# Kernel optimization log

Measured on AMD Instinct MI355X. Metric: run time of the kernel, lower is better.

Reference implementation:

```python
import jax, jax.numpy as jnp
import numpy as np

B = 4096  # number of graphs (segments)
H = 256   # hidden_aff = hidden_comp = hidden_prot
NEG = -1e30

def leaky(x):
    return jax.nn.leaky_relu(x, 0.1)

def _lin(key, fin, fout):
    k1, k2 = jax.random.split(key)
    lim = 1.0 / np.sqrt(fin)
    W = jax.random.uniform(k1, (fin, fout), jnp.float32, -lim, lim)
    b = jax.random.uniform(k2, (fout,), jnp.float32, -lim, lim)
    return W, b

def setup_inputs() -> dict:
    key = jax.random.key(0)
    ks = jax.random.split(key, 16)
    N = 262144
    comp_feature = jax.random.normal(ks[0], (N, H), jnp.float32)
    prot_feature = jax.random.normal(ks[1], (N, H), jnp.float32)
    batch_comp = jnp.sort(jax.random.randint(ks[2], (N,), 0, B, jnp.int32))
    batch_prot = jnp.sort(jax.random.randint(ks[3], (N,), 0, B, jnp.int32))
    c_aff_W, c_aff_b = _lin(ks[4], H, H)
    c_sup_W, c_sup_b = _lin(ks[5], H, H)
    p_aff_W, p_aff_b = _lin(ks[6], H, H)
    raw_W1, raw_b1 = _lin(ks[7], 3 * H, H)
    raw_W2, raw_b2 = _lin(ks[8], H, H)
    alpha_W1, alpha_b1 = _lin(ks[9], 3 * H, H)
    alpha_W2, alpha_b2 = _lin(ks[10], H, 1)
    out_W1, out_b1 = _lin(ks[11], H, H)
    out_W2, out_b2 = _lin(ks[12], H, 1)
    return dict(comp_feature=comp_feature, prot_feature=prot_feature,
                batch_comp=batch_comp, batch_prot=batch_prot,
                c_aff_W=c_aff_W, c_aff_b=c_aff_b, c_sup_W=c_sup_W, c_sup_b=c_sup_b,
                p_aff_W=p_aff_W, p_aff_b=p_aff_b,
                raw_W1=raw_W1, raw_b1=raw_b1, raw_W2=raw_W2, raw_b2=raw_b2,
                alpha_W1=alpha_W1, alpha_b1=alpha_b1, alpha_W2=alpha_W2, alpha_b2=alpha_b2,
                out_W1=out_W1, out_b1=out_b1, out_W2=out_W2, out_b2=out_b2)

def reference(comp_feature, prot_feature, batch_comp, batch_prot,
              c_aff_W, c_aff_b, c_sup_W, c_sup_b, p_aff_W, p_aff_b,
              raw_W1, raw_b1, raw_W2, raw_b2,
              alpha_W1, alpha_b1, alpha_W2, alpha_b2,
              out_W1, out_b1, out_W2, out_b2):
    comp_emb = leaky(comp_feature @ c_aff_W + c_aff_b)           # [N, H]
    prot_emb = leaky(prot_feature @ p_aff_W + p_aff_b)           # [N, H]
    prot_pool = jax.ops.segment_max(prot_emb, batch_prot, num_segments=B)  # [B, H]
    supe = jax.ops.segment_sum(leaky(comp_feature @ c_sup_W + c_sup_b),
                               batch_comp, num_segments=B)       # [B, H]
    feat = jnp.concatenate([comp_emb, supe[batch_comp], prot_pool[batch_comp]], axis=1)  # [N, 3H]
    raw = leaky(feat @ raw_W1 + raw_b1) @ raw_W2 + raw_b2        # [N, H]
    prealpha = leaky(feat @ alpha_W1 + alpha_b1) @ alpha_W2 + alpha_b2  # [N, 1]
    # scatter softmax over graphs
    seg_max = jax.ops.segment_max(prealpha, batch_comp, num_segments=B)
    a_exp = jnp.exp(prealpha - seg_max[batch_comp])
    a_sum = jax.ops.segment_sum(a_exp, batch_comp, num_segments=B) + 1e-6
    alpha = a_exp / a_sum[batch_comp]                            # [N, 1]
    vector = jax.ops.segment_sum(raw * alpha, batch_comp, num_segments=B)  # [B, H]
    affinity_pred = leaky(vector @ out_W1 + out_b1) @ out_W2 + out_b2      # [B, 1]
    return vector, alpha, affinity_pred
```

## Files before the change

kernel.cpp:

```cpp
#include <hip/hip_runtime.h>
#include <cstddef>
#include <cstdint>

#define HDIM 256
#define BSEG 4096

typedef __bf16 bf16x8 __attribute__((ext_vector_type(8)));
typedef float f32x4 __attribute__((ext_vector_type(4)));

__device__ __forceinline__ float leaky(float x) { return x >= 0.f ? x : 0.1f * x; }
__device__ __forceinline__ float bf2f(ushort u) {
    return __builtin_bit_cast(float, (uint32_t)u << 16);
}
__device__ __forceinline__ ushort f2bf(float f) {
    uint32_t x = __builtin_bit_cast(uint32_t, f);
    return (ushort)((x + 0x7fffu + ((x >> 16) & 1u)) >> 16);
}
__device__ __forceinline__ bf16x8 pack8(float4 a, float4 b) {
    union { ushort s[8]; bf16x8 v; } u;
    u.s[0] = f2bf(a.x); u.s[1] = f2bf(a.y); u.s[2] = f2bf(a.z); u.s[3] = f2bf(a.w);
    u.s[4] = f2bf(b.x); u.s[5] = f2bf(b.y); u.s[6] = f2bf(b.z); u.s[7] = f2bf(b.w);
    return u.v;
}
__device__ __forceinline__ void store_bf4(ushort* p, float v0, float v1, float v2, float v3) {
    ushort4 o; o.x = f2bf(v0); o.y = f2bf(v1); o.z = f2bf(v2); o.w = f2bf(v3);
    *(ushort4*)p = o;
}

__device__ __forceinline__ void gld16(const ushort* g, ushort* lds) {
    __builtin_amdgcn_global_load_lds(
        (const __attribute__((address_space(1))) uint32_t*)g,
        (__attribute__((address_space(3))) uint32_t*)lds, 16, 0, 0);
}

__global__ void seg_bounds_k(const int* __restrict__ bc, const int* __restrict__ bp,
                             int* __restrict__ sc, int* __restrict__ sp, int n, int nb)
{
    int t = blockIdx.x * blockDim.x + threadIdx.x;
    if (t >= 2 * (nb + 1)) return;
    bool isc = (t <= nb);
    const int* a = isc ? bc : bp;
    int v = isc ? t : t - (nb + 1);
    int lo = 0, hi = n;
    while (lo < hi) { int mid = (lo + hi) >> 1; if (a[mid] < v) lo = mid + 1; else hi = mid; }
    if (isc) sc[t] = lo; else sp[t - (nb + 1)] = lo;
}

__global__ __launch_bounds__(256) void wt_cast_all(
    const float* __restrict__ s0, const float* __restrict__ s1,
    const float* __restrict__ s2, const float* __restrict__ s3,
    const float* __restrict__ s4,
    ushort* __restrict__ d0, ushort* __restrict__ d1, ushort* __restrict__ d2,
    ushort* __restrict__ d3, ushort* __restrict__ d4)
{
    int m = blockIdx.x >> 4, tile = blockIdx.x & 15;
    const float* s = m == 0 ? s0 : m == 1 ? s1 : m == 2 ? s2 : m == 3 ? s3 : s4;
    ushort*      d = m == 0 ? d0 : m == 1 ? d1 : m == 2 ? d2 : m == 3 ? d3 : d4;
    int r0 = (tile >> 2) * 64, c0 = (tile & 3) * 64;
    __shared__ ushort t[64][72];
    int cc = threadIdx.x & 63, rr = threadIdx.x >> 6;
    for (int r = rr; r < 64; r += 4) t[cc][r] = f2bf(s[(size_t)(r0 + r) * 256 + c0 + cc]);
    __syncthreads();
    for (int r = rr; r < 64; r += 4) d[(size_t)(c0 + r) * 256 + r0 + cc] = t[r][cc];
}

template<bool LEAKYACT, bool ROWBIAS, bool AFP32, bool ALPHADOT, int YT>
__global__ __launch_bounds__(512) void mg3(
    const void* __restrict__ Av, const ushort* __restrict__ WT,
    const float* __restrict__ bias0, const float* __restrict__ bias1,
    const float* __restrict__ rt0, const float* __restrict__ rt1,
    const int* __restrict__ idx,
    ushort* __restrict__ out0, ushort* __restrict__ out1,
    const float* __restrict__ w2, float* __restrict__ pre)
{
    __shared__ __attribute__((aligned(16))) ushort Bs[2][256 * 32];
    __shared__ __attribute__((aligned(16))) ushort As[2][128 * 32];
    __shared__ float pb[128][4];

    const int tid = threadIdx.x;
    const int l = tid & 63, w = tid >> 6;

    const uint nwg = gridDim.x, orig = blockIdx.x;
    const uint swz = (orig & 7) * (nwg >> 3) + (orig >> 3);
    const int bx = (int)(swz / YT), cb = (int)(swz % YT);
    const int row0 = bx * 128, colb = cb * 256;

    const float*  Af = (const float*)Av;
    const ushort* Ah = (const ushort*)Av;

    const int sB0 = w * 128 + l;
    const int rB0 = sB0 >> 2,        rB1 = (sB0 + 64) >> 2;
    const int qB0 = (sB0 & 3) ^ ((rB0 >> 1) & 3), qB1 = ((sB0 + 64) & 3) ^ ((rB1 >> 1) & 3);
    const ushort* srcB0 = WT + (size_t)(colb + rB0) * HDIM + qB0 * 8;
    const ushort* srcB1 = WT + (size_t)(colb + rB1) * HDIM + qB1 * 8;
    const int srow = tid >> 2, sj = tid & 3;
    const int lj = sj ^ ((srow >> 1) & 3);
    const float*  fsrcA = Af + (size_t)(row0 + srow) * HDIM + lj * 8;
    const ushort* hsrcA = Ah + (size_t)(row0 + srow) * HDIM + lj * 8;

    const int wr = (w >> 2) * 64, wc = (w & 3) * 64;
    const int lr = l & 15, lt = l >> 4;

    f32x4 acc[4][4] = {};

#define STAGE_B(buf, k0) do { \
        gld16(srcB0 + (k0), &Bs[buf][sB0 * 8]); \
        gld16(srcB1 + (k0), &Bs[buf][(sB0 + 64) * 8]); \
    } while (0)

#define COMPUTE(buf) do { \
        bf16x8 af[4], bv[4]; \
        _Pragma("unroll") \
        for (int m = 0; m < 4; ++m) { \
            const int row = wr + m * 16 + lr; \
            const int q = lt ^ ((row >> 1) & 3); \
            af[m] = *(const bf16x8*)&As[buf][row * 32 + q * 8]; \
        } \
        _Pragma("unroll") \
        for (int n = 0; n < 4; ++n) { \
            const int brow = wc + n * 16 + lr; \
            const int q = lt ^ ((brow >> 1) & 3); \
            bv[n] = *(const bf16x8*)&Bs[buf][brow * 32 + q * 8]; \
        } \
        _Pragma("unroll") \
        for (int m = 0; m < 4; ++m) \
            _Pragma("unroll") \
            for (int n = 0; n < 4; ++n) \
                acc[m][n] = __builtin_amdgcn_mfma_f32_16x16x32_bf16(bv[n], af[m], acc[m][n], 0, 0, 0); \
    } while (0)

    int cur = 0;
    if (AFP32) {
        float4 av0, av1;
        av0 = *(const float4*)(fsrcA + 0);
        av1 = *(const float4*)(fsrcA + 4);
        STAGE_B(0, 0);
        *(bf16x8*)&As[0][tid * 8] = pack8(av0, av1);
        __syncthreads();
        #pragma unroll
        for (int t = 1; t < 8; ++t) {
            av0 = *(const float4*)(fsrcA + t * 32);
            av1 = *(const float4*)(fsrcA + t * 32 + 4);
            STAGE_B(cur ^ 1, t * 32);
            COMPUTE(cur);
            *(bf16x8*)&As[cur ^ 1][tid * 8] = pack8(av0, av1);
            __syncthreads();
            cur ^= 1;
        }
        COMPUTE(cur);
    } else {
        STAGE_B(0, 0);
        gld16(hsrcA, &As[0][tid * 8]);
        __syncthreads();
        #pragma unroll
        for (int t = 1; t < 8; ++t) {
            STAGE_B(cur ^ 1, t * 32);
            gld16(hsrcA + t * 32, &As[cur ^ 1][tid * 8]);
            COMPUTE(cur);
            __syncthreads();
            cur ^= 1;
        }
        COMPUTE(cur);
    }

#undef STAGE_B
#undef COMPUTE

    if (ALPHADOT && cb == 1) {
        #pragma unroll
        for (int m = 0; m < 4; ++m) {
            const int row = row0 + wr + m * 16 + lr;
            const float* rrow = rt1 + (size_t)idx[row] * HDIM;
            float p = 0.f;
            #pragma unroll
            for (int n = 0; n < 4; ++n) {
                const int c = wc + n * 16 + (lt << 2);
                float4 r4 = *(const float4*)&rrow[c];
                float4 w4 = *(const float4*)&w2[c];
                float v0 = acc[m][n][0] + r4.x, v1 = acc[m][n][1] + r4.y;
                float v2 = acc[m][n][2] + r4.z, v3 = acc[m][n][3] + r4.w;
                if (LEAKYACT) { v0 = leaky(v0); v1 = leaky(v1); v2 = leaky(v2); v3 = leaky(v3); }
                p += v0 * w4.x + v1 * w4.y + v2 * w4.z + v3 * w4.w;
            }
            p += __shfl_xor(p, 16);
            p += __shfl_xor(p, 32);
            if (lt == 0) pb[wr + m * 16 + lr][w & 3] = p;
        }
        __syncthreads();
        if (tid < 128) pre[row0 + tid] = pb[tid][0] + pb[tid][1] + pb[tid][2] + pb[tid][3];
    } else {
        const float* bias = (YT == 2 && cb == 1) ? bias1 : bias0;
        const float* rtab = (YT == 2 && cb == 1) ? rt1 : rt0;
        ushort* outp = (YT == 2 && cb == 1) ? out1 : out0;
        #pragma unroll
        for (int m = 0; m < 4; ++m) {
            const int row = row0 + wr + m * 16 + lr;
            const float* rrow = nullptr;
            if (ROWBIAS) rrow = rtab + (size_t)idx[row] * HDIM;
            #pragma unroll
            for (int n = 0; n < 4; ++n) {
                const int c = wc + n * 16 + (lt << 2);
                float v0 = acc[m][n][0], v1 = acc[m][n][1], v2 = acc[m][n][2], v3 = acc[m][n][3];
                if (bias) {
                    float4 b4 = *(const float4*)&bias[c];
                    v0 += b4.x; v1 += b4.y; v2 += b4.z; v3 += b4.w;
                }
                if (ROWBIAS) {
                    float4 r4 = *(const float4*)&rrow[c];
                    v0 += r4.x; v1 += r4.y; v2 += r4.z; v3 += r4.w;
                }
                if (LEAKYACT) { v0 = leaky(v0); v1 = leaky(v1); v2 = leaky(v2); v3 = leaky(v3); }
                store_bf4(&outp[(size_t)row * HDIM + c], v0, v1, v2, v3);
            }
        }
    }
}

__global__ __launch_bounds__(256) void gemm64_2(
    const float* __restrict__ A, const float* __restrict__ A2,
    const float* __restrict__ Wb_r, const float* __restrict__ Wc_r, const float* __restrict__ bias_r,
    const float* __restrict__ Wb_a, const float* __restrict__ Wc_a, const float* __restrict__ bias_a,
    float* __restrict__ Cr, float* __restrict__ Ca)
{
    const int K = HDIM, NO = HDIM;
    const float* W  = blockIdx.z ? Wb_a : Wb_r;
    const float* W2 = blockIdx.z ? Wc_a : Wc_r;
    const float* bias = blockIdx.z ? bias_a : bias_r;
    float* C = blockIdx.z ? Ca : Cr;

    __shared__ float As [16][68];
    __shared__ float Bs [16][68];
    __shared__ float As2[16][68];
    __shared__ float Bs2[16][68];

    const int tid = threadIdx.x;
    const int tx = tid & 15, ty = tid >> 4;
    const int row0 = blockIdx.x * 64, col0 = blockIdx.y * 64;

    const int lr = tid >> 2;
    const int lk = (tid & 3) << 2;
    const int bk = tid >> 4;
    const int bj = (tid & 15) << 2;

    float acc[4][4] = {};

    for (int k0 = 0; k0 < K; k0 += 16) {
        float4 a4 = *(const float4*)&A[(size_t)(row0 + lr) * K + k0 + lk];
        As[lk + 0][lr] = a4.x; As[lk + 1][lr] = a4.y;
        As[lk + 2][lr] = a4.z; As[lk + 3][lr] = a4.w;
        *(float4*)&Bs[bk][bj] = *(const float4*)&W[(size_t)(k0 + bk) * NO + col0 + bj];
        float4 c4 = *(const float4*)&A2[(size_t)(row0 + lr) * K + k0 + lk];
        As2[lk + 0][lr] = c4.x; As2[lk + 1][lr] = c4.y;
        As2[lk + 2][lr] = c4.z; As2[lk + 3][lr] = c4.w;
        *(float4*)&Bs2[bk][bj] = *(const float4*)&W2[(size_t)(k0 + bk) * NO + col0 + bj];
        __syncthreads();
        #pragma unroll
        for (int kk = 0; kk < 16; ++kk) {
            float4 av = *(const float4*)&As[kk][ty << 2];
            float4 bv = *(const float4*)&Bs[kk][tx << 2];
            float a_[4] = {av.x, av.y, av.z, av.w};
            float b_[4] = {bv.x, bv.y, bv.z, bv.w};
            #pragma unroll
            for (int i = 0; i < 4; ++i)
                #pragma unroll
                for (int j = 0; j < 4; ++j)
                    acc[i][j] += a_[i] * b_[j];
            float4 av2 = *(const float4*)&As2[kk][ty << 2];
            float4 bv2 = *(const float4*)&Bs2[kk][tx << 2];
            float c_[4] = {av2.x, av2.y, av2.z, av2.w};
            float d_[4] = {bv2.x, bv2.y, bv2.z, bv2.w};
            #pragma unroll
            for (int i = 0; i < 4; ++i)
                #pragma unroll
                for (int j = 0; j < 4; ++j)
                    acc[i][j] += c_[i] * d_[j];
        }
        __syncthreads();
    }

    #pragma unroll
    for (int i = 0; i < 4; ++i) {
        int row = row0 + (ty << 2) + i;
        float vv[4];
        #pragma unroll
        for (int j = 0; j < 4; ++j) {
            int col = col0 + (tx << 2) + j;
            vv[j] = acc[i][j] + bias[col];
        }
        float4 o; o.x = vv[0]; o.y = vv[1]; o.z = vv[2]; o.w = vv[3];
        *(float4*)&C[(size_t)row * NO + col0 + (tx << 2)] = o;
    }
}

template<bool ISMAX>
__global__ __launch_bounds__(256) void seg_reduce8(const ushort* __restrict__ in,
        const int* __restrict__ starts, float* __restrict__ out)
{
    __shared__ float part[8][HDIM];
    const int b = blockIdx.x, tid = threadIdx.x;
    const int sub = tid & 31, r = tid >> 5;
    const int s = starts[b], e = starts[b + 1];
    float a[8];
    #pragma unroll
    for (int j = 0; j < 8; ++j) a[j] = ISMAX ? -INFINITY : 0.f;
    for (int i = s + r; i < e; i += 8) {
        uint4 v = *(const uint4*)&in[(size_t)i * HDIM + sub * 8];
        float f[8] = { bf2f((ushort)v.x), bf2f((ushort)(v.x >> 16)),
                       bf2f((ushort)v.y), bf2f((ushort)(v.y >> 16)),
                       bf2f((ushort)v.z), bf2f((ushort)(v.z >> 16)),
                       bf2f((ushort)v.w), bf2f((ushort)(v.w >> 16)) };
        #pragma unroll
        for (int j = 0; j < 8; ++j) a[j] = ISMAX ? fmaxf(a[j], f[j]) : (a[j] + f[j]);
    }
    #pragma unroll
    for (int j = 0; j < 8; ++j) part[r][sub * 8 + j] = a[j];
    __syncthreads();
    float res = part[0][tid];
    #pragma unroll
    for (int j = 1; j < 8; ++j) res = ISMAX ? fmaxf(res, part[j][tid]) : (res + part[j][tid]);
    out[(size_t)b * HDIM + tid] = res;
}

__global__ __launch_bounds__(64) void seg_softmax_k(const float* __restrict__ pre,
        const int* __restrict__ starts, float* __restrict__ alpha, float* __restrict__ sa)
{
    int b = blockIdx.x, lane = threadIdx.x;
    int s = starts[b], e = starts[b + 1];
    float m = -INFINITY;
    for (int i = s + lane; i < e; i += 64) m = fmaxf(m, pre[i]);
    #pragma unroll
    for (int off = 32; off; off >>= 1) m = fmaxf(m, __shfl_xor(m, off));
    float S = 0.f;
    for (int i = s + lane; i < e; i += 64) S += expf(pre[i] - m);
    #pragma unroll
    for (int off = 32; off; off >>= 1) S += __shfl_xor(S, off);
    float denom = S + 1e-6f;
    if (lane == 0) sa[b] = S / denom;
    for (int i = s + lane; i < e; i += 64) alpha[i] = expf(pre[i] - m) / denom;
}

__global__ __launch_bounds__(256) void seg_wsum8(const ushort* __restrict__ raw,
        const float* __restrict__ alpha, const int* __restrict__ starts,
        float* __restrict__ vec)
{
    __shared__ float part[8][HDIM];
    const int b = blockIdx.x, tid = threadIdx.x;
    const int sub = tid & 31, r = tid >> 5;
    const int s = starts[b], e = starts[b + 1];
    float a[8] = {};
    for (int i = s + r; i < e; i += 8) {
        float al = alpha[i];
        uint4 v = *(const uint4*)&raw[(size_t)i * HDIM + sub * 8];
        a[0] += bf2f((ushort)v.x) * al;        a[1] += bf2f((ushort)(v.x >> 16)) * al;
        a[2] += bf2f((ushort)v.y) * al;        a[3] += bf2f((ushort)(v.y >> 16)) * al;
        a[4] += bf2f((ushort)v.z) * al;        a[5] += bf2f((ushort)(v.z >> 16)) * al;
        a[6] += bf2f((ushort)v.w) * al;        a[7] += bf2f((ushort)(v.w >> 16)) * al;
    }
    #pragma unroll
    for (int j = 0; j < 8; ++j) part[r][sub * 8 + j] = a[j];
    __syncthreads();
    float res = 0.f;
    #pragma unroll
    for (int j = 0; j < 8; ++j) res += part[j][tid];
    vec[(size_t)b * HDIM + tid] = res;
}

__global__ __launch_bounds__(256) void final_k(
    const float* __restrict__ hw, const float* __restrict__ sa,
    const float* __restrict__ W2r, const float* __restrict__ rb2,
    const float* __restrict__ oW1, const float* __restrict__ ob1,
    const float* __restrict__ oW2, const float* __restrict__ ob2,
    float* __restrict__ out_vec, float* __restrict__ out_aff)
{
    __shared__ float v[HDIM];
    __shared__ float vecs[HDIM];
    __shared__ float red[4];
    int b = blockIdx.x, t = threadIdx.x;
    v[t] = hw[(size_t)b * HDIM + t];
    __syncthreads();
    float a = rb2[t] * sa[b];
    #pragma unroll 8
    for (int k = 0; k < HDIM; ++k) a += v[k] * W2r[(size_t)k * HDIM + t];
    out_vec[(size_t)b * HDIM + t] = a;
    vecs[t] = a;
    __syncthreads();
    float h = ob1[t];
    #pragma unroll 8
    for (int k = 0; k < HDIM; ++k) h += vecs[k] * oW1[(size_t)k * HDIM + t];
    h = leaky(h);
    float p = h * oW2[t];
    #pragma unroll
    for (int off = 32; off; off >>= 1) p += __shfl_down(p, off);
    int lane = t & 63, wid = t >> 6;
    if (lane == 0) red[wid] = p;
    __syncthreads();
    if (t == 0) out_aff[b] = red[0] + red[1] + red[2] + red[3] + ob2[0];
}

extern "C" void kernel_launch(void* const* d_in, const int* in_sizes, int n_in,
                              void* d_out, int out_size, void* d_ws, size_t ws_size,
                              hipStream_t stream)
{
    const int N = in_sizes[2];
    const int H = HDIM;
    const int B = BSEG;

    const float* comp   = (const float*)d_in[0];
    const float* prot   = (const float*)d_in[1];
    const int*   bc     = (const int*)d_in[2];
    const int*   bp     = (const int*)d_in[3];
    const float* c_aff_W = (const float*)d_in[4];
    const float* c_aff_b = (const float*)d_in[5];
    const float* c_sup_W = (const float*)d_in[6];
    const float* c_sup_b = (const float*)d_in[7];
    const float* p_aff_W = (const float*)d_in[8];
    const float* p_aff_b = (const float*)d_in[9];
    const float* raw_W1  = (const float*)d_in[10];
    const float* raw_b1  = (const float*)d_in[11];
    const float* raw_W2  = (const float*)d_in[12];
    const float* raw_b2  = (const float*)d_in[13];
    const float* alpha_W1 = (const float*)d_in[14];
    const float* alpha_b1 = (const float*)d_in[15];
    const float* alpha_W2 = (const float*)d_in[16];
    const float* out_W1  = (const float*)d_in[18];
    const float* out_b1  = (const float*)d_in[19];
    const float* out_W2  = (const float*)d_in[20];
    const float* out_b2  = (const float*)d_in[21];

    const size_t NBIG = (size_t)N * H;
    const size_t SSEG = (size_t)B * H;

    char* p = (char*)d_ws;
    ushort* e1 = (ushort*)p; p += NBIG * 2;
    ushort* e2 = (ushort*)p; p += NBIG * 2;
    ushort* e3 = (ushort*)p; p += NBIG * 2;
    float* supe = (float*)p;  p += SSEG * 4;
    float* pool = (float*)p;  p += SSEG * 4;
    float* gr   = (float*)p;  p += SSEG * 4;
    float* ga   = (float*)p;  p += SSEG * 4;
    float* hw   = (float*)p;  p += SSEG * 4;
    float* sa   = (float*)p;  p += (size_t)B * 4;
    float* pre  = (float*)p;  p += (size_t)N * 4;
    ushort* WT1 = (ushort*)p; p += (size_t)512 * 256 * 2;
    ushort* WTp = (ushort*)p; p += (size_t)256 * 256 * 2;
    ushort* WT2 = (ushort*)p; p += (size_t)512 * 256 * 2;
    int* sc = (int*)p; p += (size_t)(B + 1) * 4;
    int* sp = (int*)p; p += (size_t)(B + 1) * 4;
    if ((size_t)(p - (char*)d_ws) > ws_size) return;

    ushort* h1 = e3;

    float* out_vec   = (float*)d_out;
    float* out_alpha = out_vec + SSEG;
    float* out_aff   = out_alpha + N;

    dim3 blk(256), blk5(512);

    seg_bounds_k<<<(2 * (B + 1) + 255) / 256, blk, 0, stream>>>(bc, bp, sc, sp, N, B);
    wt_cast_all<<<5 * 16, blk, 0, stream>>>(
        c_aff_W, c_sup_W, p_aff_W, raw_W1, alpha_W1,
        WT1, WT1 + 65536, WTp, WT2, WT2 + 65536);

    mg3<true, false, true, false, 2><<<dim3(N / 128 * 2), blk5, 0, stream>>>(
        comp, WT1, c_aff_b, c_sup_b, nullptr, nullptr, nullptr, e1, e2, nullptr, nullptr);
    mg3<true, false, true, false, 1><<<dim3(N / 128), blk5, 0, stream>>>(
        prot, WTp, p_aff_b, nullptr, nullptr, nullptr, nullptr, e3, nullptr, nullptr, nullptr);
    seg_reduce8<false><<<B, blk, 0, stream>>>(e2, sc, supe);
    seg_reduce8<true ><<<B, blk, 0, stream>>>(e3, sp, pool);
    gemm64_2<<<dim3(B / 64, 4, 2), blk, 0, stream>>>(supe, pool,
        raw_W1 + H * H, raw_W1 + 2 * H * H, raw_b1,
        alpha_W1 + H * H, alpha_W1 + 2 * H * H, alpha_b1, gr, ga);
    mg3<true, true, false, true, 2><<<dim3(N / 128 * 2), blk5, 0, stream>>>(
        e1, WT2, nullptr, nullptr, gr, ga, bc, h1, nullptr, alpha_W2, pre);
    seg_softmax_k<<<B, dim3(64), 0, stream>>>(pre, sc, out_alpha, sa);
    seg_wsum8<<<B, blk, 0, stream>>>(h1, out_alpha, sc, hw);
    final_k<<<B, blk, 0, stream>>>(hw, sa, raw_W2, raw_b2,
        out_W1, out_b1, out_W2, out_b2, out_vec, out_aff);
}
```

Baseline: 686.3 us.

## Merge comp/prot GEMM launches and triple-buffer the K loop with depth-2 prefetch

```diff
diff --git a/kernel.cpp b/kernel.cpp
--- a/kernel.cpp
+++ b/kernel.cpp
@@ -65,16 +65,18 @@
 }
 
 template<bool LEAKYACT, bool ROWBIAS, bool AFP32, bool ALPHADOT, int YT>
-__global__ __launch_bounds__(512) void mg3(
-    const void* __restrict__ Av, const ushort* __restrict__ WT,
+__global__ __launch_bounds__(512) void mg4(
+    const void* __restrict__ Av, const void* __restrict__ Av2,
+    const ushort* __restrict__ WT,
     const float* __restrict__ bias0, const float* __restrict__ bias1,
+    const float* __restrict__ bias2,
     const float* __restrict__ rt0, const float* __restrict__ rt1,
     const int* __restrict__ idx,
-    ushort* __restrict__ out0, ushort* __restrict__ out1,
+    ushort* __restrict__ out0, ushort* __restrict__ out1, ushort* __restrict__ out2,
     const float* __restrict__ w2, float* __restrict__ pre)
 {
-    __shared__ __attribute__((aligned(16))) ushort Bs[2][256 * 32];
-    __shared__ __attribute__((aligned(16))) ushort As[2][128 * 32];
+    __shared__ __attribute__((aligned(16))) ushort Bs[3][256 * 32];
+    __shared__ __attribute__((aligned(16))) ushort As[3][128 * 32];
     __shared__ float pb[128][4];
 
     const int tid = threadIdx.x;
@@ -85,8 +87,9 @@
     const int bx = (int)(swz / YT), cb = (int)(swz % YT);
     const int row0 = bx * 128, colb = cb * 256;
 
-    const float*  Af = (const float*)Av;
-    const ushort* Ah = (const ushort*)Av;
+    const void* Asel = (YT == 3 && cb == 2) ? Av2 : Av;
+    const float*  Af = (const float*)Asel;
+    const ushort* Ah = (const ushort*)Asel;
 
     const int sB0 = w * 128 + l;
     const int rB0 = sB0 >> 2,        rB1 = (sB0 + 64) >> 2;
@@ -102,8 +105,15 @@
     const int lr = l & 15, lt = l >> 4;
 
     f32x4 acc[4][4] = {};
-
-#define STAGE_B(buf, k0) do { \
+    float4 ra[2][2];
+
+#define PREF(buf, k0, slot) do { \
+        if (AFP32) { \
+            ra[slot][0] = *(const float4*)(fsrcA + (k0)); \
+            ra[slot][1] = *(const float4*)(fsrcA + (k0) + 4); \
+        } else { \
+            gld16(hsrcA + (k0), &As[buf][tid * 8]); \
+        } \
         gld16(srcB0 + (k0), &Bs[buf][sB0 * 8]); \
         gld16(srcB1 + (k0), &Bs[buf][(sB0 + 64) * 8]); \
     } while (0)
@@ -129,41 +139,39 @@
                 acc[m][n] = __builtin_amdgcn_mfma_f32_16x16x32_bf16(bv[n], af[m], acc[m][n], 0, 0, 0); \
     } while (0)
 
-    int cur = 0;
+    PREF(0, 0, 0);
+    PREF(1, 32, 1);
     if (AFP32) {
-        float4 av0, av1;
-        av0 = *(const float4*)(fsrcA + 0);
-        av1 = *(const float4*)(fsrcA + 4);
-        STAGE_B(0, 0);
-        *(bf16x8*)&As[0][tid * 8] = pack8(av0, av1);
-        __syncthreads();
-        #pragma unroll
-        for (int t = 1; t < 8; ++t) {
-            av0 = *(const float4*)(fsrcA + t * 32);
-            av1 = *(const float4*)(fsrcA + t * 32 + 4);
-            STAGE_B(cur ^ 1, t * 32);
-            COMPUTE(cur);
-            *(bf16x8*)&As[cur ^ 1][tid * 8] = pack8(av0, av1);
-            __syncthreads();
-            cur ^= 1;
+        asm volatile("s_waitcnt vmcnt(4)" ::: "memory");
+        *(bf16x8*)&As[0][tid * 8] = pack8(ra[0][0], ra[0][1]);
+        asm volatile("s_waitcnt lgkmcnt(0)" ::: "memory");
+    } else {
+        asm volatile("s_waitcnt vmcnt(3)" ::: "memory");
+    }
+    __builtin_amdgcn_s_barrier();
+    __builtin_amdgcn_sched_barrier(0);
+
+    #pragma unroll
+    for (int t = 0; t < 8; ++t) {
+        if (t + 2 < 8) PREF((t + 2) % 3, (t + 2) * 32, t & 1);
+        COMPUTE(t % 3);
+        if (t < 7) {
+            if (t + 2 < 8) {
+                if (AFP32) asm volatile("s_waitcnt vmcnt(4)" ::: "memory");
+                else       asm volatile("s_waitcnt vmcnt(3)" ::: "memory");
+            } else {
+                asm volatile("s_waitcnt vmcnt(0)" ::: "memory");
+            }
+            if (AFP32) {
+                *(bf16x8*)&As[(t + 1) % 3][tid * 8] = pack8(ra[(t + 1) & 1][0], ra[(t + 1) & 1][1]);
+                asm volatile("s_waitcnt lgkmcnt(0)" ::: "memory");
+            }
+            __builtin_amdgcn_s_barrier();
+            __builtin_amdgcn_sched_barrier(0);
         }
-        COMPUTE(cur);
-    } else {
-        STAGE_B(0, 0);
-        gld16(hsrcA, &As[0][tid * 8]);
-        __syncthreads();
-        #pragma unroll
-        for (int t = 1; t < 8; ++t) {
-            STAGE_B(cur ^ 1, t * 32);
-            gld16(hsrcA + t * 32, &As[cur ^ 1][tid * 8]);
-            COMPUTE(cur);
-            __syncthreads();
-            cur ^= 1;
-        }
-        COMPUTE(cur);
-    }
-
-#undef STAGE_B
+    }
+
+#undef PREF
 #undef COMPUTE
 
     if (ALPHADOT && cb == 1) {
@@ -189,9 +197,9 @@
         __syncthreads();
         if (tid < 128) pre[row0 + tid] = pb[tid][0] + pb[tid][1] + pb[tid][2] + pb[tid][3];
     } else {
-        const float* bias = (YT == 2 && cb == 1) ? bias1 : bias0;
-        const float* rtab = (YT == 2 && cb == 1) ? rt1 : rt0;
-        ushort* outp = (YT == 2 && cb == 1) ? out1 : out0;
+        const float* bias = (YT >= 2 && cb == 1) ? bias1 : (YT == 3 && cb == 2) ? bias2 : bias0;
+        ushort* outp      = (YT >= 2 && cb == 1) ? out1  : (YT == 3 && cb == 2) ? out2  : out0;
+        const float* rtab = (cb == 1) ? rt1 : rt0;
         #pragma unroll
         for (int m = 0; m < 4; ++m) {
             const int row = row0 + wr + m * 16 + lr;
@@ -461,17 +469,17 @@
         c_aff_W, c_sup_W, p_aff_W, raw_W1, alpha_W1,
         WT1, WT1 + 65536, WTp, WT2, WT2 + 65536);
 
-    mg3<true, false, true, false, 2><<<dim3(N / 128 * 2), blk5, 0, stream>>>(
-        comp, WT1, c_aff_b, c_sup_b, nullptr, nullptr, nullptr, e1, e2, nullptr, nullptr);
-    mg3<true, false, true, false, 1><<<dim3(N / 128), blk5, 0, stream>>>(
-        prot, WTp, p_aff_b, nullptr, nullptr, nullptr, nullptr, e3, nullptr, nullptr, nullptr);
+    mg4<true, false, true, false, 3><<<dim3(N / 128 * 3), blk5, 0, stream>>>(
+        comp, prot, WT1, c_aff_b, c_sup_b, p_aff_b, nullptr, nullptr, nullptr,
+        e1, e2, e3, nullptr, nullptr);
     seg_reduce8<false><<<B, blk, 0, stream>>>(e2, sc, supe);
     seg_reduce8<true ><<<B, blk, 0, stream>>>(e3, sp, pool);
     gemm64_2<<<dim3(B / 64, 4, 2), blk, 0, stream>>>(supe, pool,
         raw_W1 + H * H, raw_W1 + 2 * H * H, raw_b1,
         alpha_W1 + H * H, alpha_W1 + 2 * H * H, alpha_b1, gr, ga);
-    mg3<true, true, false, true, 2><<<dim3(N / 128 * 2), blk5, 0, stream>>>(
-        e1, WT2, nullptr, nullptr, gr, ga, bc, h1, nullptr, alpha_W2, pre);
+    mg4<true, true, false, true, 2><<<dim3(N / 128 * 2), blk5, 0, stream>>>(
+        e1, nullptr, WT2, nullptr, nullptr, nullptr, gr, ga, bc,
+        h1, nullptr, nullptr, alpha_W2, pre);
     seg_softmax_k<<<B, dim3(64), 0, stream>>>(pre, sc, out_alpha, sa);
     seg_wsum8<<<B, blk, 0, stream>>>(h1, out_alpha, sc, hw);
     final_k<<<B, blk, 0, stream>>>(hw, sa, raw_W2, raw_b2,
```

Result: no change. 695.1 us (+1.3%).

## Stage full-K A tile in LDS and compute all output columns per block

Applied to the files above, without the earlier changes.

```diff
diff --git a/kernel.cpp b/kernel.cpp
--- a/kernel.cpp
+++ b/kernel.cpp
@@ -64,155 +64,148 @@
     for (int r = rr; r < 64; r += 4) d[(size_t)(c0 + r) * 256 + r0 + cc] = t[r][cc];
 }
 
-template<bool LEAKYACT, bool ROWBIAS, bool AFP32, bool ALPHADOT, int YT>
-__global__ __launch_bounds__(512) void mg3(
-    const void* __restrict__ Av, const ushort* __restrict__ WT,
-    const float* __restrict__ bias0, const float* __restrict__ bias1,
+__device__ __forceinline__ void tile_mma(const ushort* As, const ushort* __restrict__ WT,
+        int colT, int lr, int lt, f32x4 acc[4][4])
+{
+    #pragma unroll
+    for (int ks = 0; ks < 8; ++ks) {
+        bf16x8 af[4], bv[4];
+        #pragma unroll
+        for (int m = 0; m < 4; ++m) {
+            const int r = m * 16 + lr;
+            const int c = ks * 4 + lt;
+            af[m] = *(const bf16x8*)&As[(r * 32 + (c ^ (r & 7))) * 8];
+        }
+        #pragma unroll
+        for (int n = 0; n < 4; ++n)
+            bv[n] = *(const bf16x8*)&WT[(size_t)(colT + n * 16 + lr) * HDIM + ks * 32 + lt * 8];
+        #pragma unroll
+        for (int m = 0; m < 4; ++m)
+            #pragma unroll
+            for (int n = 0; n < 4; ++n)
+                acc[m][n] = __builtin_amdgcn_mfma_f32_16x16x32_bf16(bv[n], af[m], acc[m][n], 0, 0, 0);
+    }
+}
+
+template<int MODE>
+__global__ __launch_bounds__(256, 4) void mgs(
+    const float* __restrict__ Ac, const float* __restrict__ Ap,
+    const ushort* __restrict__ Ahb,
+    const ushort* __restrict__ WT,
+    const float* __restrict__ b0, const float* __restrict__ b1, const float* __restrict__ b2,
     const float* __restrict__ rt0, const float* __restrict__ rt1,
     const int* __restrict__ idx,
-    ushort* __restrict__ out0, ushort* __restrict__ out1,
-    const float* __restrict__ w2, float* __restrict__ pre)
-{
-    __shared__ __attribute__((aligned(16))) ushort Bs[2][256 * 32];
-    __shared__ __attribute__((aligned(16))) ushort As[2][128 * 32];
-    __shared__ float pb[128][4];
+    ushort* __restrict__ o0, ushort* __restrict__ o1, ushort* __restrict__ o2,
+    const float* __restrict__ w2, float* __restrict__ pre, int NB)
+{
+    __shared__ __attribute__((aligned(16))) ushort As[64 * 256];
+    __shared__ float pb[64][4];
 
     const int tid = threadIdx.x;
     const int l = tid & 63, w = tid >> 6;
-
-    const uint nwg = gridDim.x, orig = blockIdx.x;
-    const uint swz = (orig & 7) * (nwg >> 3) + (orig >> 3);
-    const int bx = (int)(swz / YT), cb = (int)(swz % YT);
-    const int row0 = bx * 128, colb = cb * 256;
-
-    const float*  Af = (const float*)Av;
-    const ushort* Ah = (const ushort*)Av;
-
-    const int sB0 = w * 128 + l;
-    const int rB0 = sB0 >> 2,        rB1 = (sB0 + 64) >> 2;
-    const int qB0 = (sB0 & 3) ^ ((rB0 >> 1) & 3), qB1 = ((sB0 + 64) & 3) ^ ((rB1 >> 1) & 3);
-    const ushort* srcB0 = WT + (size_t)(colb + rB0) * HDIM + qB0 * 8;
-    const ushort* srcB1 = WT + (size_t)(colb + rB1) * HDIM + qB1 * 8;
-    const int srow = tid >> 2, sj = tid & 3;
-    const int lj = sj ^ ((srow >> 1) & 3);
-    const float*  fsrcA = Af + (size_t)(row0 + srow) * HDIM + lj * 8;
-    const ushort* hsrcA = Ah + (size_t)(row0 + srow) * HDIM + lj * 8;
-
-    const int wr = (w >> 2) * 64, wc = (w & 3) * 64;
     const int lr = l & 15, lt = l >> 4;
 
-    f32x4 acc[4][4] = {};
-
-#define STAGE_B(buf, k0) do { \
-        gld16(srcB0 + (k0), &Bs[buf][sB0 * 8]); \
-        gld16(srcB1 + (k0), &Bs[buf][(sB0 + 64) * 8]); \
-    } while (0)
-
-#define COMPUTE(buf) do { \
-        bf16x8 af[4], bv[4]; \
-        _Pragma("unroll") \
-        for (int m = 0; m < 4; ++m) { \
-            const int row = wr + m * 16 + lr; \
-            const int q = lt ^ ((row >> 1) & 3); \
-            af[m] = *(const bf16x8*)&As[buf][row * 32 + q * 8]; \
-        } \
-        _Pragma("unroll") \
-        for (int n = 0; n < 4; ++n) { \
-            const int brow = wc + n * 16 + lr; \
-            const int q = lt ^ ((brow >> 1) & 3); \
-            bv[n] = *(const bf16x8*)&Bs[buf][brow * 32 + q * 8]; \
-        } \
-        _Pragma("unroll") \
-        for (int m = 0; m < 4; ++m) \
-            _Pragma("unroll") \
-            for (int n = 0; n < 4; ++n) \
-                acc[m][n] = __builtin_amdgcn_mfma_f32_16x16x32_bf16(bv[n], af[m], acc[m][n], 0, 0, 0); \
-    } while (0)
-
-    int cur = 0;
-    if (AFP32) {
-        float4 av0, av1;
-        av0 = *(const float4*)(fsrcA + 0);
-        av1 = *(const float4*)(fsrcA + 4);
-        STAGE_B(0, 0);
-        *(bf16x8*)&As[0][tid * 8] = pack8(av0, av1);
+    const int bid = blockIdx.x;
+    const bool isProt = (MODE == 0) && (bid >= NB);
+    const int row0 = (isProt ? bid - NB : bid) * 64;
+
+    if (MODE == 0) {
+        const float* A = isProt ? Ap : Ac;
+        #pragma unroll
+        for (int i = 0; i < 8; ++i) {
+            const int s = i * 256 + tid;
+            const int r = s >> 5, q = s & 31;
+            const float* src = A + (size_t)(row0 + r) * HDIM + ((q ^ (r & 7)) << 3);
+            float4 x = *(const float4*)src;
+            float4 y = *(const float4*)(src + 4);
+            *(bf16x8*)&As[s * 8] = pack8(x, y);
+        }
+    } else {
+        #pragma unroll
+        for (int i = 0; i < 8; ++i) {
+            const int s = i * 256 + tid;
+            const int r = s >> 5, q = s & 31;
+            gld16(Ahb + (size_t)(row0 + r) * HDIM + ((q ^ (r & 7)) << 3), &As[s * 8]);
+        }
+    }
+    __syncthreads();
+
+    if (MODE == 0) {
+        const int ntile = isProt ? 1 : 2;
+        #pragma unroll
+        for (int t = 0; t < 2; ++t) {
+            if (t >= ntile) break;
+            const int colT = isProt ? (512 + w * 64) : (w * 128 + t * 64);
+            f32x4 acc[4][4] = {};
+            tile_mma(As, WT, colT, lr, lt, acc);
+            const int g = colT >> 8;
+            const float* bias = g == 0 ? b0 : g == 1 ? b1 : b2;
+            ushort* outp      = g == 0 ? o0 : g == 1 ? o1 : o2;
+            const int cin = (colT & 255) + (lt << 2);
+            #pragma unroll
+            for (int m = 0; m < 4; ++m) {
+                const int row = row0 + m * 16 + lr;
+                #pragma unroll
+                for (int n = 0; n < 4; ++n) {
+                    const int c = cin + n * 16;
+                    float4 b4 = *(const float4*)&bias[c];
+                    float v0 = leaky(acc[m][n][0] + b4.x);
+                    float v1 = leaky(acc[m][n][1] + b4.y);
+                    float v2 = leaky(acc[m][n][2] + b4.z);
+                    float v3 = leaky(acc[m][n][3] + b4.w);
+                    store_bf4(&outp[(size_t)row * HDIM + c], v0, v1, v2, v3);
+                }
+            }
+        }
+    } else {
+        {
+            const int colT = w * 64;
+            f32x4 acc[4][4] = {};
+            tile_mma(As, WT, colT, lr, lt, acc);
+            const int cin = colT + (lt << 2);
+            #pragma unroll
+            for (int m = 0; m < 4; ++m) {
+                const int row = row0 + m * 16 + lr;
+                const float* rrow = rt0 + (size_t)idx[row] * HDIM;
+                #pragma unroll
+                for (int n = 0; n < 4; ++n) {
+                    const int c = cin + n * 16;
+                    float4 r4 = *(const float4*)&rrow[c];
+                    float v0 = leaky(acc[m][n][0] + r4.x);
+                    float v1 = leaky(acc[m][n][1] + r4.y);
+                    float v2 = leaky(acc[m][n][2] + r4.z);
+                    float v3 = leaky(acc[m][n][3] + r4.w);
+                    store_bf4(&o0[(size_t)row * HDIM + c], v0, v1, v2, v3);
+                }
+            }
+        }
+        {
+            const int colT = 256 + w * 64;
+            f32x4 acc[4][4] = {};
+            tile_mma(As, WT, colT, lr, lt, acc);
+            const int cin = (colT - 256) + (lt << 2);
+            #pragma unroll
+            for (int m = 0; m < 4; ++m) {
+                const int row = row0 + m * 16 + lr;
+                const float* rrow = rt1 + (size_t)idx[row] * HDIM;
+                float p = 0.f;
+                #pragma unroll
+                for (int n = 0; n < 4; ++n) {
+                    const int c = cin + n * 16;
+                    float4 r4 = *(const float4*)&rrow[c];
+                    float4 w4 = *(const float4*)&w2[c];
+                    p += leaky(acc[m][n][0] + r4.x) * w4.x;
+                    p += leaky(acc[m][n][1] + r4.y) * w4.y;
+                    p += leaky(acc[m][n][2] + r4.z) * w4.z;
+                    p += leaky(acc[m][n][3] + r4.w) * w4.w;
+                }
+                p += __shfl_xor(p, 16);
+                p += __shfl_xor(p, 32);
+                if (lt == 0) pb[m * 16 + lr][w] = p;
+            }
+        }
         __syncthreads();
-        #pragma unroll
-        for (int t = 1; t < 8; ++t) {
-            av0 = *(const float4*)(fsrcA + t * 32);
-            av1 = *(const float4*)(fsrcA + t * 32 + 4);
-            STAGE_B(cur ^ 1, t * 32);
-            COMPUTE(cur);
-            *(bf16x8*)&As[cur ^ 1][tid * 8] = pack8(av0, av1);
-            __syncthreads();
-            cur ^= 1;
-        }
-        COMPUTE(cur);
-    } else {
-        STAGE_B(0, 0);
-        gld16(hsrcA, &As[0][tid * 8]);
-        __syncthreads();
-        #pragma unroll
-        for (int t = 1; t < 8; ++t) {
-            STAGE_B(cur ^ 1, t * 32);
-            gld16(hsrcA + t * 32, &As[cur ^ 1][tid * 8]);
-            COMPUTE(cur);
-            __syncthreads();
-            cur ^= 1;
-        }
-        COMPUTE(cur);
-    }
-
-#undef STAGE_B
-#undef COMPUTE
-
-    if (ALPHADOT && cb == 1) {
-        #pragma unroll
-        for (int m = 0; m < 4; ++m) {
-            const int row = row0 + wr + m * 16 + lr;
-            const float* rrow = rt1 + (size_t)idx[row] * HDIM;
-            float p = 0.f;
-            #pragma unroll
-            for (int n = 0; n < 4; ++n) {
-                const int c = wc + n * 16 + (lt << 2);
-                float4 r4 = *(const float4*)&rrow[c];
-                float4 w4 = *(const float4*)&w2[c];
-                float v0 = acc[m][n][0] + r4.x, v1 = acc[m][n][1] + r4.y;
-                float v2 = acc[m][n][2] + r4.z, v3 = acc[m][n][3] + r4.w;
-                if (LEAKYACT) { v0 = leaky(v0); v1 = leaky(v1); v2 = leaky(v2); v3 = leaky(v3); }
-                p += v0 * w4.x + v1 * w4.y + v2 * w4.z + v3 * w4.w;
-            }
-            p += __shfl_xor(p, 16);
-            p += __shfl_xor(p, 32);
-            if (lt == 0) pb[wr + m * 16 + lr][w & 3] = p;
-        }
-        __syncthreads();
-        if (tid < 128) pre[row0 + tid] = pb[tid][0] + pb[tid][1] + pb[tid][2] + pb[tid][3];
-    } else {
-        const float* bias = (YT == 2 && cb == 1) ? bias1 : bias0;
-        const float* rtab = (YT == 2 && cb == 1) ? rt1 : rt0;
-        ushort* outp = (YT == 2 && cb == 1) ? out1 : out0;
-        #pragma unroll
-        for (int m = 0; m < 4; ++m) {
-            const int row = row0 + wr + m * 16 + lr;
-            const float* rrow = nullptr;
-            if (ROWBIAS) rrow = rtab + (size_t)idx[row] * HDIM;
-            #pragma unroll
-            for (int n = 0; n < 4; ++n) {
-                const int c = wc + n * 16 + (lt << 2);
-                float v0 = acc[m][n][0], v1 = acc[m][n][1], v2 = acc[m][n][2], v3 = acc[m][n][3];
-                if (bias) {
-                    float4 b4 = *(const float4*)&bias[c];
-                    v0 += b4.x; v1 += b4.y; v2 += b4.z; v3 += b4.w;
-                }
-                if (ROWBIAS) {
-                    float4 r4 = *(const float4*)&rrow[c];
-                    v0 += r4.x; v1 += r4.y; v2 += r4.z; v3 += r4.w;
-                }
-                if (LEAKYACT) { v0 = leaky(v0); v1 = leaky(v1); v2 = leaky(v2); v3 = leaky(v3); }
-                store_bf4(&outp[(size_t)row * HDIM + c], v0, v1, v2, v3);
-            }
-        }
+        if (tid < 64) pre[row0 + tid] = pb[tid][0] + pb[tid][1] + pb[tid][2] + pb[tid][3];
     }
 }
 
@@ -454,24 +447,25 @@
     float* out_alpha = out_vec + SSEG;
     float* out_aff   = out_alpha + N;
 
-    dim3 blk(256), blk5(512);
+    dim3 blk(256);
+    const int NB = N / 64;
 
     seg_bounds_k<<<(2 * (B + 1) + 255) / 256, blk, 0, stream>>>(bc, bp, sc, sp, N, B);
     wt_cast_all<<<5 * 16, blk, 0, stream>>>(
         c_aff_W, c_sup_W, p_aff_W, raw_W1, alpha_W1,
         WT1, WT1 + 65536, WTp, WT2, WT2 + 65536);
 
-    mg3<true, false, true, false, 2><<<dim3(N / 128 * 2), blk5, 0, stream>>>(
-        comp, WT1, c_aff_b, c_sup_b, nullptr, nullptr, nullptr, e1, e2, nullptr, nullptr);
-    mg3<true, false, true, false, 1><<<dim3(N / 128), blk5, 0, stream>>>(
-        prot, WTp, p_aff_b, nullptr, nullptr, nullptr, nullptr, e3, nullptr, nullptr, nullptr);
+    mgs<0><<<2 * NB, blk, 0, stream>>>(
+        comp, prot, nullptr, WT1, c_aff_b, c_sup_b, p_aff_b,
+        nullptr, nullptr, nullptr, e1, e2, e3, nullptr, nullptr, NB);
     seg_reduce8<false><<<B, blk, 0, stream>>>(e2, sc, supe);
     seg_reduce8<true ><<<B, blk, 0, stream>>>(e3, sp, pool);
     gemm64_2<<<dim3(B / 64, 4, 2), blk, 0, stream>>>(supe, pool,
         raw_W1 + H * H, raw_W1 + 2 * H * H, raw_b1,
         alpha_W1 + H * H, alpha_W1 + 2 * H * H, alpha_b1, gr, ga);
-    mg3<true, true, false, true, 2><<<dim3(N / 128 * 2), blk5, 0, stream>>>(
-        e1, WT2, nullptr, nullptr, gr, ga, bc, h1, nullptr, alpha_W2, pre);
+    mgs<1><<<NB, blk, 0, stream>>>(
+        nullptr, nullptr, e1, WT2, nullptr, nullptr, nullptr,
+        gr, ga, bc, h1, nullptr, nullptr, alpha_W2, pre, NB);
     seg_softmax_k<<<B, dim3(64), 0, stream>>>(pre, sc, out_alpha, sa);
     seg_wsum8<<<B, blk, 0, stream>>>(h1, out_alpha, sc, hw);
     final_k<<<B, blk, 0, stream>>>(hw, sa, raw_W2, raw_b2,
```

After: 749.7 us. 9.2% more time.

## Prefetch A two stages ahead with manual vmcnt waits in GEMM main loop

Applied to the files above, without the earlier changes.

```diff
diff --git a/kernel.cpp b/kernel.cpp
--- a/kernel.cpp
+++ b/kernel.cpp
@@ -65,7 +65,7 @@
 }
 
 template<bool LEAKYACT, bool ROWBIAS, bool AFP32, bool ALPHADOT, int YT>
-__global__ __launch_bounds__(512) void mg3(
+__global__ __launch_bounds__(512) void mg5(
     const void* __restrict__ Av, const ushort* __restrict__ WT,
     const float* __restrict__ bias0, const float* __restrict__ bias1,
     const float* __restrict__ rt0, const float* __restrict__ rt1,
@@ -102,11 +102,29 @@
     const int lr = l & 15, lt = l >> 4;
 
     f32x4 acc[4][4] = {};
+    float4 fa0[2], fa1[2];
+    bf16x8 ha[2];
 
 #define STAGE_B(buf, k0) do { \
         gld16(srcB0 + (k0), &Bs[buf][sB0 * 8]); \
         gld16(srcB1 + (k0), &Bs[buf][(sB0 + 64) * 8]); \
     } while (0)
+
+#define LOAD_A(slot, k0) do { \
+        if (AFP32) { \
+            fa0[slot] = *(const float4*)(fsrcA + (k0)); \
+            fa1[slot] = *(const float4*)(fsrcA + (k0) + 4); \
+        } else { \
+            ha[slot] = *(const bf16x8*)(hsrcA + (k0)); \
+        } \
+    } while (0)
+
+#define WRITE_A(buf, slot) do { \
+        if (AFP32) *(bf16x8*)&As[buf][tid * 8] = pack8(fa0[slot], fa1[slot]); \
+        else       *(bf16x8*)&As[buf][tid * 8] = ha[slot]; \
+    } while (0)
+
+#define FENCE asm volatile("" ::: "memory")
 
 #define COMPUTE(buf) do { \
         bf16x8 af[4], bv[4]; \
@@ -129,41 +147,40 @@
                 acc[m][n] = __builtin_amdgcn_mfma_f32_16x16x32_bf16(bv[n], af[m], acc[m][n], 0, 0, 0); \
     } while (0)
 
-    int cur = 0;
-    if (AFP32) {
-        float4 av0, av1;
-        av0 = *(const float4*)(fsrcA + 0);
-        av1 = *(const float4*)(fsrcA + 4);
-        STAGE_B(0, 0);
-        *(bf16x8*)&As[0][tid * 8] = pack8(av0, av1);
-        __syncthreads();
-        #pragma unroll
-        for (int t = 1; t < 8; ++t) {
-            av0 = *(const float4*)(fsrcA + t * 32);
-            av1 = *(const float4*)(fsrcA + t * 32 + 4);
-            STAGE_B(cur ^ 1, t * 32);
-            COMPUTE(cur);
-            *(bf16x8*)&As[cur ^ 1][tid * 8] = pack8(av0, av1);
-            __syncthreads();
-            cur ^= 1;
+    LOAD_A(0, 0);
+    FENCE;
+    STAGE_B(0, 0);
+    FENCE;
+    LOAD_A(1, 32);
+    FENCE;
+    WRITE_A(0, 0);
+    if (AFP32) asm volatile("s_waitcnt vmcnt(2) lgkmcnt(0)" ::: "memory");
+    else       asm volatile("s_waitcnt vmcnt(1) lgkmcnt(0)" ::: "memory");
+    __builtin_amdgcn_s_barrier();
+
+    #pragma unroll
+    for (int t = 0; t < 8; ++t) {
+        if (t < 7) STAGE_B((t + 1) & 1, (t + 1) * 32);
+        FENCE;
+        if (t < 6) LOAD_A(t & 1, (t + 2) * 32);
+        FENCE;
+        COMPUTE(t & 1);
+        if (t < 7) {
+            WRITE_A((t + 1) & 1, (t + 1) & 1);
+            if (t < 6) {
+                if (AFP32) asm volatile("s_waitcnt vmcnt(2) lgkmcnt(0)" ::: "memory");
+                else       asm volatile("s_waitcnt vmcnt(1) lgkmcnt(0)" ::: "memory");
+            } else {
+                asm volatile("s_waitcnt vmcnt(0) lgkmcnt(0)" ::: "memory");
+            }
+            __builtin_amdgcn_s_barrier();
         }
-        COMPUTE(cur);
-    } else {
-        STAGE_B(0, 0);
-        gld16(hsrcA, &As[0][tid * 8]);
-        __syncthreads();
-        #pragma unroll
-        for (int t = 1; t < 8; ++t) {
-            STAGE_B(cur ^ 1, t * 32);
-            gld16(hsrcA + t * 32, &As[cur ^ 1][tid * 8]);
-            COMPUTE(cur);
-            __syncthreads();
-            cur ^= 1;
-        }
-        COMPUTE(cur);
     }
 
 #undef STAGE_B
+#undef LOAD_A
+#undef WRITE_A
+#undef FENCE
 #undef COMPUTE
 
     if (ALPHADOT && cb == 1) {
@@ -461,16 +478,16 @@
         c_aff_W, c_sup_W, p_aff_W, raw_W1, alpha_W1,
         WT1, WT1 + 65536, WTp, WT2, WT2 + 65536);
 
-    mg3<true, false, true, false, 2><<<dim3(N / 128 * 2), blk5, 0, stream>>>(
+    mg5<true, false, true, false, 2><<<dim3(N / 128 * 2), blk5, 0, stream>>>(
         comp, WT1, c_aff_b, c_sup_b, nullptr, nullptr, nullptr, e1, e2, nullptr, nullptr);
-    mg3<true, false, true, false, 1><<<dim3(N / 128), blk5, 0, stream>>>(
+    mg5<true, false, true, false, 1><<<dim3(N / 128), blk5, 0, stream>>>(
         prot, WTp, p_aff_b, nullptr, nullptr, nullptr, nullptr, e3, nullptr, nullptr, nullptr);
     seg_reduce8<false><<<B, blk, 0, stream>>>(e2, sc, supe);
     seg_reduce8<true ><<<B, blk, 0, stream>>>(e3, sp, pool);
     gemm64_2<<<dim3(B / 64, 4, 2), blk, 0, stream>>>(supe, pool,
         raw_W1 + H * H, raw_W1 + 2 * H * H, raw_b1,
         alpha_W1 + H * H, alpha_W1 + 2 * H * H, alpha_b1, gr, ga);
-    mg3<true, true, false, true, 2><<<dim3(N / 128 * 2), blk5, 0, stream>>>(
+    mg5<true, true, false, true, 2><<<dim3(N / 128 * 2), blk5, 0, stream>>>(
         e1, WT2, nullptr, nullptr, gr, ga, bc, h1, nullptr, alpha_W2, pre);
     seg_softmax_k<<<B, dim3(64), 0, stream>>>(pre, sc, out_alpha, sa);
     seg_wsum8<<<B, blk, 0, stream>>>(h1, out_alpha, sc, hw);
```

Measured after the change: 702.8 us. 1.02x slower.
